# Kernel optimization log

Measured on AMD Instinct MI355X. Metric: run time of the kernel, lower is better.

## Reference

```python
import jax, jax.numpy as jnp
import numpy as np

N_NODES = 50000
N_EDGES = 800000
NODE_DIM = 64
EDGE_DIM = 16
HID = 64
HEADS = 4
LAYERS = 3
N_GRAPHS = 32
N_QUERY = 4096
BN_EPS = 1e-5
LRELU_SLOPE = 0.2


def setup_inputs() -> dict:
    key = jax.random.key(0)
    ks = jax.random.split(key, 20)
    s = 0.1  # weight scale
    return {
        "node_feat": jax.random.normal(ks[0], (N_NODES, NODE_DIM), jnp.float32),
        "edge_feat": jax.random.normal(ks[1], (N_EDGES, EDGE_DIM), jnp.float32),
        "node_proj_w": jax.random.normal(ks[2], (NODE_DIM, HID), jnp.float32) * s,
        "node_proj_b": jax.random.normal(ks[3], (HID,), jnp.float32) * s,
        "edge_proj_w": jax.random.normal(ks[4], (EDGE_DIM, HID), jnp.float32) * s,
        "edge_proj_b": jax.random.normal(ks[5], (HID,), jnp.float32) * s,
        "fc_w": jax.random.normal(ks[6], (LAYERS, HID, HEADS * HID), jnp.float32) * s,
        "fc_edge_w": jax.random.normal(ks[7], (LAYERS, HID, HEADS * HID), jnp.float32) * s,
        "attn_l": jax.random.normal(ks[8], (LAYERS, HEADS, HID), jnp.float32) * s,
        "attn_r": jax.random.normal(ks[9], (LAYERS, HEADS, HID), jnp.float32) * s,
        "attn_e": jax.random.normal(ks[10], (LAYERS, HEADS, HID), jnp.float32) * s,
        "conv_bias": jax.random.normal(ks[11], (LAYERS, HEADS * HID), jnp.float32) * s,
        "bn_gamma": jnp.ones((LAYERS, HID), jnp.float32),
        "bn_beta": jnp.zeros((LAYERS, HID), jnp.float32),
        "head_w": jax.random.normal(ks[12], (HEADS * HID, HID), jnp.float32) * s,
        "head_b": jax.random.normal(ks[13], (HID,), jnp.float32) * s,
        "src": jax.random.randint(ks[14], (N_EDGES,), 0, N_NODES, jnp.int64 if jax.config.jax_enable_x64 else jnp.int32),
        "dst": jax.random.randint(ks[15], (N_EDGES,), 0, N_NODES, jnp.int64 if jax.config.jax_enable_x64 else jnp.int32),
        "graph_ids": jnp.sort(jax.random.randint(ks[16], (N_NODES,), 0, N_GRAPHS)),
        "nodes_idx": jax.random.randint(ks[17], (N_QUERY,), 0, N_NODES),
        "num_graphs": N_GRAPHS,
    }


def reference(node_feat, edge_feat, node_proj_w, node_proj_b, edge_proj_w,
              edge_proj_b, fc_w, fc_edge_w, attn_l, attn_r, attn_e, conv_bias,
              bn_gamma, bn_beta, head_w, head_b, src, dst, graph_ids,
              nodes_idx, num_graphs):
    N = node_feat.shape[0]
    L, H, D = attn_l.shape

    nodes = node_feat @ node_proj_w + node_proj_b        # (N, hid)
    edges = edge_feat @ edge_proj_w + edge_proj_b        # (E, hid)

    x = None
    for l in range(L):
        # NOTE: faithful to original -- every layer consumes the ORIGINAL
        # projected node features (output is never fed back into `nodes`).
        ft = (nodes @ fc_w[l]).reshape(N, H, D)          # (N, H, D)
        fe = (edges @ fc_edge_w[l]).reshape(-1, H, D)    # (E, H, D)
        el = jnp.einsum('nhd,hd->nh', ft, attn_l[l])     # (N, H)
        er = jnp.einsum('nhd,hd->nh', ft, attn_r[l])
        ee = jnp.einsum('ehd,hd->eh', fe, attn_e[l])     # (E, H)
        e = jax.nn.leaky_relu(el[src] + er[dst] + ee, LRELU_SLOPE)
        # edge softmax over incoming edges of each destination node
        emax = jax.ops.segment_max(e, dst, num_segments=N)
        ex = jnp.exp(e - emax[dst])
        denom = jax.ops.segment_sum(ex, dst, num_segments=N)
        a = ex / denom[dst]                              # (E, H)
        # message = a * (feat_src + feat_edge), scatter-sum to dst
        m = a[:, :, None] * (ft[src] + fe)               # (E, H, D)
        rst = jax.ops.segment_sum(m, dst, num_segments=N)  # (N, H, D)
        rst = jax.nn.silu(rst + conv_bias[l].reshape(H, D))
        # BatchNorm1d(hidden) after permute(0,2,1): channel dim is D,
        # stats over (N, H). Training-mode batch statistics.
        mean = rst.mean(axis=(0, 1))
        var = rst.var(axis=(0, 1))
        x = (rst - mean) * jax.lax.rsqrt(var + BN_EPS) * bn_gamma[l] + bn_beta[l]

    x = x.reshape(N, H * D) @ head_w + head_b            # (N, hid)

    ones = jnp.ones((N, 1), x.dtype)
    sums = jax.ops.segment_sum(x, graph_ids, num_segments=num_graphs)
    counts = jax.ops.segment_sum(ones, graph_ids, num_segments=num_graphs)
    pooled = sums / jnp.maximum(counts, 1.0)             # (G, hid)
    return pooled, x[nodes_idx]
```

## Files before the change

### kernel.cpp

```cpp
#include <hip/hip_runtime.h>
#include <cstdint>
#include <cstddef>

#define N_NODES 50000
#define N_EDGES 800000
#define HID 64
#define HEADS 4
#define N_GRAPHS 32
#define N_QUERY 4096
#define N_TILES 3125
#define N_CBLK  782

typedef unsigned short ushort_t;
typedef unsigned int uint_t;
typedef __attribute__((ext_vector_type(8))) short short8_t;
typedef __attribute__((ext_vector_type(4))) float f32x4_t;

__device__ __forceinline__ float b2f(ushort_t h) { return __uint_as_float(((uint_t)h) << 16); }
__device__ __forceinline__ ushort_t f2b(float f) {
    uint_t u = __float_as_uint(f);
    uint_t r = (u + 0x7FFFu + ((u >> 16) & 1u)) >> 16;
    return (ushort_t)r;
}

static constexpr size_t OFF_DEG   = 0;
static constexpr size_t OFF_GST   = 50016;
static constexpr size_t OFF_OFFS  = 50064;
static constexpr size_t OFF_RANK  = 100080;
static constexpr size_t OFF_AL    = 900080;
static constexpr size_t OFF_AR    = 900336;
static constexpr size_t OFF_B     = 900592;
static constexpr size_t OFF_CE    = 900656;
static constexpr size_t OFF_CB    = 900672;
static constexpr size_t OFF_SS    = 900928;
static constexpr size_t OFF_HB2   = 901056;
static constexpr size_t OFF_WQE   = 901120;
static constexpr size_t OFF_WCVT  = 905216;
static constexpr size_t OFF_WHT   = 946176;
static constexpr size_t OFF_EL    = 954368;
static constexpr size_t OFF_ER    = 1154368;
static constexpr size_t OFF_NB    = 1354368;
static constexpr size_t OFF_REC   = 2954368;
static constexpr size_t OFF_U     = 6154624;
static constexpr size_t OFF_RST   = 14154624;
static constexpr size_t OFF_X     = 20554624;
static constexpr size_t OFF_SCR   = 23754624;
static constexpr size_t OFF_SCR2  = 24154624;
static constexpr size_t WS_TOTAL  = 24171008;

__global__ void setup1_kernel(const float* __restrict__ fcw2, const float* __restrict__ fcew2,
                              const float* __restrict__ attl2, const float* __restrict__ attr2,
                              const float* __restrict__ atte2,
                              const float* __restrict__ wpe, const float* __restrict__ bpe,
                              const int* __restrict__ gids,
                              float* __restrict__ Al, float* __restrict__ Ar,
                              float* __restrict__ B, float* __restrict__ Ce,
                              float* __restrict__ Cb, float* __restrict__ Wqe,
                              int* __restrict__ gstart)
{
    int b = blockIdx.x, tid = threadIdx.x;
    if (b == 0) {
        __shared__ float AE[256];
        int c = tid >> 2, h = tid & 3;
        float al = 0.f, ar = 0.f, ae = 0.f;
        for (int d = 0; d < 64; d++) {
            float wl = fcw2[c*256 + h*64 + d];
            float we = fcew2[c*256 + h*64 + d];
            al = fmaf(wl, attl2[h*64 + d], al);
            ar = fmaf(wl, attr2[h*64 + d], ar);
            ae = fmaf(we, atte2[h*64 + d], ae);
        }
        Al[c*4 + h] = al;
        Ar[c*4 + h] = ar;
        AE[c*4 + h] = ae;
        __syncthreads();
        if (tid < 64) {
            int kk = tid >> 2, hh = tid & 3;
            float bb = 0.f;
            for (int d = 0; d < 64; d++) bb = fmaf(wpe[kk*64 + d], AE[d*4 + hh], bb);
            B[kk*4 + hh] = bb;
        }
        if (tid < 4) {
            float ce = 0.f;
            for (int d = 0; d < 64; d++) ce = fmaf(bpe[d], AE[d*4 + tid], ce);
            Ce[tid] = ce;
        }
        {
            float cb = 0.f;
            for (int d = 0; d < 64; d++) cb = fmaf(bpe[d], fcew2[d*256 + tid], cb);
            Cb[tid] = cb;
        }
    } else if (b <= 16) {
        int idx = (b - 1) * 256 + tid;
        int hh = idx >> 10, rem = idx & 1023, kk = rem >> 6, cc = rem & 63;
        float w = 0.f;
        for (int d = 0; d < 64; d++) w = fmaf(wpe[kk*64 + d], fcew2[d*256 + hh*64 + cc], w);
        Wqe[idx] = w;
    } else {
        int g = tid;
        if (g <= N_GRAPHS) {
            int lo = 0, hi = N_NODES;
            while (lo < hi) { int mid = (lo + hi) >> 1; if (gids[mid] < g) lo = mid + 1; else hi = mid; }
            gstart[g] = lo;
        }
    }
}

__global__ void wcvt_kernel(const float* __restrict__ fcw2, const float* __restrict__ Wqe,
                            ushort_t* __restrict__ wcvt)
{
    int idx = blockIdx.x * 256 + threadIdx.x;
    int kt = idx >> 8, col = idx & 255;
    int hc = col >> 6;
    short8_t v8;
#pragma unroll
    for (int j = 0; j < 8; j++) {
        int k = kt*8 + j;
        float v;
        if (k < 256) {
            v = ((k >> 6) == hc) ? fcw2[(size_t)(k & 63)*256 + col] : 0.f;
        } else {
            int kq = k - 256, hh = kq >> 4;
            v = (hh == hc) ? Wqe[hh*1024 + (kq & 15)*64 + (col & 63)] : 0.f;
        }
        v8[j] = (short)f2b(v);
    }
    *(short8_t*)&wcvt[(size_t)idx*8] = v8;
}

__global__ __launch_bounds__(256) void node_proj_kernel(
    const float* __restrict__ nf, const float* __restrict__ wp, const float* __restrict__ bpn,
    const float* __restrict__ Al, const float* __restrict__ Ar,
    ushort_t* __restrict__ nb, float* __restrict__ el, float* __restrict__ er)
{
    __shared__ float rows[4][64];
    int tid = threadIdx.x, w = tid >> 6, lane = tid & 63;
    int n = blockIdx.x * 4 + w;
    rows[w][lane] = nf[(size_t)n*64 + lane];
    __syncthreads();
    float acc = bpn[lane];
    for (int k = 0; k < 64; k++) acc = fmaf(rows[w][k], wp[k*64 + lane], acc);
    nb[(size_t)n*64 + lane] = f2b(acc);
    float pl[4], pr[4];
#pragma unroll
    for (int h = 0; h < 4; h++) { pl[h] = acc * Al[lane*4 + h]; pr[h] = acc * Ar[lane*4 + h]; }
#pragma unroll
    for (int off = 32; off > 0; off >>= 1) {
#pragma unroll
        for (int h = 0; h < 4; h++) {
            pl[h] += __shfl_xor(pl[h], off, 64);
            pr[h] += __shfl_xor(pr[h], off, 64);
        }
    }
    if (lane == 0) {
#pragma unroll
        for (int h = 0; h < 4; h++) { el[(size_t)n*4 + h] = pl[h]; er[(size_t)n*4 + h] = pr[h]; }
    }
}

__global__ void hist_kernel(const int* __restrict__ dst, int* __restrict__ deg,
                            int* __restrict__ rank)
{
    int e = blockIdx.x * 256 + threadIdx.x;
    if (e < N_EDGES) rank[e] = atomicAdd(&deg[dst[e]], 1);
}

__global__ __launch_bounds__(1024) void prefix_kernel(const int* __restrict__ deg,
                                                      int* __restrict__ offs)
{
    __shared__ int wsum[16];
    __shared__ int carry_s;
    int tid = threadIdx.x, lane = tid & 63, w = tid >> 6;
    if (tid == 0) carry_s = 0;
    __syncthreads();
    for (int base = 0; base < N_NODES; base += 1024) {
        int i = base + tid;
        int v = (i < N_NODES) ? deg[i] : 0;
        int incl = v;
#pragma unroll
        for (int off = 1; off < 64; off <<= 1) {
            int y = __shfl_up(incl, off, 64);
            if (lane >= off) incl += y;
        }
        if (lane == 63) wsum[w] = incl;
        __syncthreads();
        int c0 = carry_s;
        int woff = 0;
#pragma unroll
        for (int k = 0; k < 15; k++) woff += (k < w) ? wsum[k] : 0;
        int ex = c0 + woff + incl - v;
        if (i < N_NODES) offs[i] = ex;
        __syncthreads();
        if (tid == 1023) carry_s = c0 + woff + incl;
        __syncthreads();
    }
    if (tid == 0) offs[N_NODES] = carry_s;
}

__global__ __launch_bounds__(256) void logit_kernel(
    const int* __restrict__ rank, const int* __restrict__ offs,
    const int* __restrict__ src, const int* __restrict__ dst,
    const float* __restrict__ edge_feat, const float* __restrict__ el,
    const float* __restrict__ B, const float* __restrict__ Ce,
    int4* __restrict__ rec)
{
    int e = blockIdx.x * 256 + threadIdx.x;
    if (e >= N_EDGES) return;
    int sn = src[e], dn = dst[e];
    const float4* el4 = (const float4*)el;
    float4 a = el4[sn];
    float l0 = Ce[0] + a.x;
    float l1 = Ce[1] + a.y;
    float l2 = Ce[2] + a.z;
    float l3 = Ce[3] + a.w;
    const float4* ef4 = (const float4*)(edge_feat + (size_t)e * 16);
    float4 e0 = ef4[0], e1 = ef4[1], e2 = ef4[2], e3 = ef4[3];
    float ef[16] = {e0.x,e0.y,e0.z,e0.w, e1.x,e1.y,e1.z,e1.w,
                    e2.x,e2.y,e2.z,e2.w, e3.x,e3.y,e3.z,e3.w};
#pragma unroll
    for (int k = 0; k < 16; k++) {
        float f = ef[k];
        l0 = fmaf(f, B[k*4 + 0], l0);
        l1 = fmaf(f, B[k*4 + 1], l1);
        l2 = fmaf(f, B[k*4 + 2], l2);
        l3 = fmaf(f, B[k*4 + 3], l3);
    }
    int slot = offs[dn] + rank[e];
    uint_t lo01 = (uint_t)f2b(l0) | ((uint_t)f2b(l1) << 16);
    uint_t lo23 = (uint_t)f2b(l2) | ((uint_t)f2b(l3) << 16);
    rec[slot] = make_int4((int)lo01, (int)lo23, sn, e);
}

__global__ __launch_bounds__(256) void accum_kernel(
    const int* __restrict__ offs, const int4* __restrict__ rec,
    const float* __restrict__ er, const float* __restrict__ edge_feat,
    const ushort_t* __restrict__ nb, ushort_t* __restrict__ u)
{
    int tid = threadIdx.x;
    int lane = tid & 63;
    int li = lane & 15;
    int node = blockIdx.x * 16 + (tid >> 6) * 4 + ((lane >> 4) & 3);
    int start = offs[node], end = offs[node + 1];
    int deg = end - start;

    float4 er4 = *(const float4*)&er[(size_t)node*4];
    const int4 Z4 = make_int4(0, 0, 0, 0);
    int4 r0 = (li < deg)      ? rec[start + li]      : Z4;
    int4 r1 = (16 + li < deg) ? rec[start + 16 + li] : Z4;

    float pe0[4], pe1[4];
    {
        float l[4] = { b2f((ushort_t)((uint_t)r0.x & 0xffff)) + er4.x,
                       b2f((ushort_t)((uint_t)r0.x >> 16))    + er4.y,
                       b2f((ushort_t)((uint_t)r0.y & 0xffff)) + er4.z,
                       b2f((ushort_t)((uint_t)r0.y >> 16))    + er4.w };
#pragma unroll
        for (int h = 0; h < 4; h++) {
            float lv = (l[h] > 0.f) ? l[h] : 0.2f * l[h];
            pe0[h] = (li < deg) ? __expf(lv) : 0.f;
        }
    }
    {
        float l[4] = { b2f((ushort_t)((uint_t)r1.x & 0xffff)) + er4.x,
                       b2f((ushort_t)((uint_t)r1.x >> 16))    + er4.y,
                       b2f((ushort_t)((uint_t)r1.y & 0xffff)) + er4.z,
                       b2f((ushort_t)((uint_t)r1.y >> 16))    + er4.w };
#pragma unroll
        for (int h = 0; h < 4; h++) {
            float lv = (l[h] > 0.f) ? l[h] : 0.2f * l[h];
            pe1[h] = (16 + li < deg) ? __expf(lv) : 0.f;
        }
    }
    int sn0 = r0.z, eid0 = r0.w;
    int sn1 = r1.z, eid1 = r1.w;

    int mdeg = deg;
#pragma unroll
    for (int off = 1; off < 64; off <<= 1) mdeg = max(mdeg, __shfl_xor(mdeg, off, 64));
    mdeg = __builtin_amdgcn_readfirstlane(mdeg);

    float z0 = 0.f, z1 = 0.f, z2 = 0.f, z3 = 0.f;
    float t[4][4] = {{0.f}};
    float q[4] = {0.f, 0.f, 0.f, 0.f};
    int grpbase = lane & 48;

#pragma unroll 2
    for (int j = 0; j < mdeg; ++j) {
        bool act = j < deg;
        float a0, a1, a2, a3;
        int sn, eid;
        if (j < 32) {
            float v0 = (j < 16) ? pe0[0] : pe1[0];
            float v1 = (j < 16) ? pe0[1] : pe1[1];
            float v2 = (j < 16) ? pe0[2] : pe1[2];
            float v3 = (j < 16) ? pe0[3] : pe1[3];
            int vs = (j < 16) ? sn0 : sn1;
            int ve = (j < 16) ? eid0 : eid1;
            int sl = grpbase | (j & 15);
            a0 = __shfl(v0, sl, 64);
            a1 = __shfl(v1, sl, 64);
            a2 = __shfl(v2, sl, 64);
            a3 = __shfl(v3, sl, 64);
            sn  = __shfl(vs, sl, 64);
            eid = __shfl(ve, sl, 64);
        } else {
            a0 = a1 = a2 = a3 = 0.f;
            sn = 0; eid = 0;
            if (act) {
                int4 rr = rec[start + j];
                float l0 = b2f((ushort_t)((uint_t)rr.x & 0xffff)) + er4.x;
                float l1 = b2f((ushort_t)((uint_t)rr.x >> 16))    + er4.y;
                float l2 = b2f((ushort_t)((uint_t)rr.y & 0xffff)) + er4.z;
                float l3 = b2f((ushort_t)((uint_t)rr.y >> 16))    + er4.w;
                l0 = (l0 > 0.f) ? l0 : 0.2f * l0;
                l1 = (l1 > 0.f) ? l1 : 0.2f * l1;
                l2 = (l2 > 0.f) ? l2 : 0.2f * l2;
                l3 = (l3 > 0.f) ? l3 : 0.2f * l3;
                a0 = __expf(l0); a1 = __expf(l1); a2 = __expf(l2); a3 = __expf(l3);
                sn = rr.z; eid = rr.w;
            }
        }
        z0 += a0; z1 += a1; z2 += a2; z3 += a3;
        ushort4 nv = *(const ushort4*)&nb[(size_t)sn*64 + li*4];
        float nd0 = b2f(nv.x), nd1 = b2f(nv.y), nd2 = b2f(nv.z), nd3 = b2f(nv.w);
        t[0][0] = fmaf(a0, nd0, t[0][0]); t[0][1] = fmaf(a0, nd1, t[0][1]);
        t[0][2] = fmaf(a0, nd2, t[0][2]); t[0][3] = fmaf(a0, nd3, t[0][3]);
        t[1][0] = fmaf(a1, nd0, t[1][0]); t[1][1] = fmaf(a1, nd1, t[1][1]);
        t[1][2] = fmaf(a1, nd2, t[1][2]); t[1][3] = fmaf(a1, nd3, t[1][3]);
        t[2][0] = fmaf(a2, nd0, t[2][0]); t[2][1] = fmaf(a2, nd1, t[2][1]);
        t[2][2] = fmaf(a2, nd2, t[2][2]); t[2][3] = fmaf(a2, nd3, t[2][3]);
        t[3][0] = fmaf(a3, nd0, t[3][0]); t[3][1] = fmaf(a3, nd1, t[3][1]);
        t[3][2] = fmaf(a3, nd2, t[3][2]); t[3][3] = fmaf(a3, nd3, t[3][3]);
        float efv = edge_feat[(size_t)eid*16 + li];
        q[0] = fmaf(a0, efv, q[0]);
        q[1] = fmaf(a1, efv, q[1]);
        q[2] = fmaf(a2, efv, q[2]);
        q[3] = fmaf(a3, efv, q[3]);
    }

    float zinv[4];
    zinv[0] = (z0 > 0.f) ? 1.f / z0 : 0.f;
    zinv[1] = (z1 > 0.f) ? 1.f / z1 : 0.f;
    zinv[2] = (z2 > 0.f) ? 1.f / z2 : 0.f;
    zinv[3] = (z3 > 0.f) ? 1.f / z3 : 0.f;

    ushort_t* up = u + (size_t)node * 320;
#pragma unroll
    for (int h = 0; h < 4; h++) {
        ushort4 tv;
        tv.x = f2b(t[h][0] * zinv[h]); tv.y = f2b(t[h][1] * zinv[h]);
        tv.z = f2b(t[h][2] * zinv[h]); tv.w = f2b(t[h][3] * zinv[h]);
        *(ushort4*)&up[h*64 + li*4] = tv;
        up[256 + h*16 + li] = f2b(q[h] * zinv[h]);
    }
}

__global__ __launch_bounds__(256) void conv_kernel(
    const ushort_t* __restrict__ u, const ushort_t* __restrict__ wcvt,
    const float* __restrict__ Cb, const float* __restrict__ convb2,
    const int* __restrict__ offs, ushort_t* __restrict__ rst, float* __restrict__ scr)
{
    int tid = threadIdx.x, lane = tid & 63;
    int li = lane & 15, lg = lane >> 4;
    int tile = blockIdx.x * 4 + (tid >> 6);
    if (tile >= N_TILES) return;
    int n0 = tile * 16;

    f32x4_t acc[16];
#pragma unroll
    for (int cb = 0; cb < 16; cb++) acc[cb] = (f32x4_t){0.f, 0.f, 0.f, 0.f};
    const ushort_t* urow = u + (size_t)(n0 + li) * 320 + lg * 8;
    const ushort_t* wbase = wcvt + ((size_t)lg * 256 + li) * 8;

#pragma unroll
    for (int kt = 0; kt < 10; kt++) {
        short8_t a = *(const short8_t*)(urow + kt * 32);
        const ushort_t* wk = wbase + (size_t)kt * 8192;
        short8_t b[16];
#pragma unroll
        for (int cb = 0; cb < 16; cb++)
            b[cb] = *(const short8_t*)(wk + (size_t)cb * 128);
#pragma unroll
        for (int cb = 0; cb < 16; cb++)
            acc[cb] = __builtin_amdgcn_mfma_f32_16x16x32_bf16(a, b[cb], acc[cb], 0, 0, 0);
    }

    float fl4[4];
#pragma unroll
    for (int j = 0; j < 4; j++) {
        int n = n0 + lg*4 + j;
        fl4[j] = (offs[n+1] > offs[n]) ? 1.f : 0.f;
    }
    float ds[4] = {0.f, 0.f, 0.f, 0.f};
    float dsq[4] = {0.f, 0.f, 0.f, 0.f};
#pragma unroll
    for (int cb = 0; cb < 16; cb++) {
        int col = cb*16 + li;
        float bias = convb2[col];
        float cbv  = Cb[col];
        float s = 0.f, sq = 0.f;
#pragma unroll
        for (int j = 0; j < 4; j++) {
            float v = acc[cb][j] + bias + fl4[j] * cbv;
            float r = v / (1.f + __expf(-v));
            rst[(size_t)(n0 + lg*4 + j)*256 + col] = f2b(r);
            s += r; sq += r * r;
        }
        s  += __shfl_xor(s, 16, 64);  s  += __shfl_xor(s, 32, 64);
        sq += __shfl_xor(sq, 16, 64); sq += __shfl_xor(sq, 32, 64);
        ds[cb & 3]  += s;
        dsq[cb & 3] += sq;
    }
    if (lg == 0) {
        float* sp = scr + (size_t)tile * 128;
#pragma unroll
        for (int m = 0; m < 4; m++) {
            sp[m*16 + li]      = ds[m];
            sp[64 + m*16 + li] = dsq[m];
        }
    }
}

__global__ __launch_bounds__(128) void scr_reduce_kernel(const float* __restrict__ scr,
                                                         float* __restrict__ scr2)
{
    int b = blockIdx.x, tid = threadIdx.x;
    float s = 0.f;
    for (int r = b; r < N_TILES; r += 128) s += scr[(size_t)r*128 + tid];
    scr2[(size_t)b*128 + tid] = s;
}

__global__ void bn_finalize_kernel(const float* __restrict__ scr2, const float* __restrict__ gamma2,
                                   const float* __restrict__ beta2, float* __restrict__ ss)
{
    __shared__ float part[8][128];
    __shared__ float tot[128];
    int j = threadIdx.x & 127, chunk = threadIdx.x >> 7;
    float t = 0.f;
    for (int b = chunk; b < 128; b += 8) t += scr2[(size_t)b*128 + j];
    part[chunk][j] = t;
    __syncthreads();
    if (threadIdx.x < 128) {
        float sgm = 0.f;
        for (int c = 0; c < 8; c++) sgm += part[c][threadIdx.x];
        tot[threadIdx.x] = sgm;
    }
    __syncthreads();
    if (threadIdx.x < 64) {
        float inv = 1.f / (float)(N_NODES * HEADS);
        float mean = tot[threadIdx.x] * inv;
        float var  = tot[64 + threadIdx.x] * inv - mean * mean;
        float sc = gamma2[threadIdx.x] * rsqrtf(var + 1e-5f);
        ss[threadIdx.x]      = sc;
        ss[64 + threadIdx.x] = beta2[threadIdx.x] - mean * sc;
    }
}

__global__ void head_prep_kernel(const float* __restrict__ ss, const float* __restrict__ headw,
                                 const float* __restrict__ headb,
                                 ushort_t* __restrict__ wht, float* __restrict__ hb2)
{
    int b = blockIdx.x, tid = threadIdx.x;
    if (b < 64) {
        int idx = b * 256 + tid;
        int c = idx >> 8, k = idx & 255;
        wht[(size_t)((k >> 3)*64 + c)*8 + (k & 7)] = f2b(ss[k & 63] * headw[(size_t)k*64 + c]);
    } else if (tid < 64) {
        float s = headb[tid];
        for (int k = 0; k < 256; k++) s += ss[64 + (k & 63)] * headw[(size_t)k*64 + tid];
        hb2[tid] = s;
    }
}

__global__ __launch_bounds__(512) void head_kernel(
    const ushort_t* __restrict__ rst, const ushort_t* __restrict__ wht,
    const float* __restrict__ hb2, float* __restrict__ x)
{
    __shared__ ushort_t Bs[16384];
    int tid = threadIdx.x, w = tid >> 6, lane = tid & 63;
    int li = lane & 15, lg = lane >> 4;
    int tile = blockIdx.x * 8 + w;
    bool active = tile < N_TILES;
    int n0 = tile * 16;

#pragma unroll
    for (int s = 0; s < 4; s++) {
        int i = tid + s*512;
        *(short8_t*)&Bs[(size_t)i*8] = *(const short8_t*)(wht + (size_t)i*8);
    }
    __syncthreads();

    if (!active) return;
    f32x4_t acc[4];
#pragma unroll
    for (int cb = 0; cb < 4; cb++) acc[cb] = (f32x4_t){0.f, 0.f, 0.f, 0.f};
    const ushort_t* rrow = rst + (size_t)(n0 + li) * 256 + lg * 8;
#pragma unroll
    for (int kt = 0; kt < 8; kt++) {
        short8_t a = *(const short8_t*)(rrow + kt * 32);
        short8_t b[4];
#pragma unroll
        for (int cb = 0; cb < 4; cb++)
            b[cb] = *(const short8_t*)&Bs[(size_t)((kt*4 + lg)*64 + cb*16 + li)*8];
#pragma unroll
        for (int cb = 0; cb < 4; cb++)
            acc[cb] = __builtin_amdgcn_mfma_f32_16x16x32_bf16(a, b[cb], acc[cb], 0, 0, 0);
    }
#pragma unroll
    for (int cb = 0; cb < 4; cb++) {
        int col = cb*16 + li;
        float hb = hb2[col];
#pragma unroll
        for (int j = 0; j < 4; j++)
            x[(size_t)(n0 + lg*4 + j)*64 + col] = acc[cb][j] + hb;
    }
}

__global__ __launch_bounds__(1024) void pool_kernel(const float* __restrict__ x,
                                                    const int* __restrict__ gstart,
                                                    float* __restrict__ out)
{
    __shared__ float red[16][64];
    int g = blockIdx.x;
    int lane = threadIdx.x & 63, w = threadIdx.x >> 6;
    int s = gstart[g], e = gstart[g + 1];
    float acc = 0.f;
    for (int n = s + w; n < e; n += 16) acc += x[(size_t)n*64 + lane];
    red[w][lane] = acc;
    __syncthreads();
    if (w == 0) {
        float t = 0.f;
#pragma unroll
        for (int k = 0; k < 16; k++) t += red[k][lane];
        float c = (float)(e - s);
        out[(size_t)g*64 + lane] = t / fmaxf(c, 1.f);
    }
}

__global__ void gather_kernel(const float* __restrict__ x, const int* __restrict__ nidx,
                              float* __restrict__ outq)
{
    int i = blockIdx.x * 256 + threadIdx.x;
    if (i < N_QUERY * HID) {
        int q = i >> 6, c = i & 63;
        outq[i] = x[(size_t)nidx[q]*64 + c];
    }
}

extern "C" void kernel_launch(void* const* d_in, const int* in_sizes, int n_in,
                              void* d_out, int out_size, void* d_ws, size_t ws_size,
                              hipStream_t stream)
{
    const float* node_feat   = (const float*)d_in[0];
    const float* edge_feat   = (const float*)d_in[1];
    const float* node_proj_w = (const float*)d_in[2];
    const float* node_proj_b = (const float*)d_in[3];
    const float* edge_proj_w = (const float*)d_in[4];
    const float* edge_proj_b = (const float*)d_in[5];
    const float* fc_w        = (const float*)d_in[6];
    const float* fc_edge_w   = (const float*)d_in[7];
    const float* attn_l      = (const float*)d_in[8];
    const float* attn_r      = (const float*)d_in[9];
    const float* attn_e      = (const float*)d_in[10];
    const float* conv_bias   = (const float*)d_in[11];
    const float* bn_gamma    = (const float*)d_in[12];
    const float* bn_beta     = (const float*)d_in[13];
    const float* head_w      = (const float*)d_in[14];
    const float* head_b      = (const float*)d_in[15];
    const int*   src         = (const int*)d_in[16];
    const int*   dst         = (const int*)d_in[17];
    const int*   gids        = (const int*)d_in[18];
    const int*   nidx        = (const int*)d_in[19];

    if (ws_size < WS_TOTAL * sizeof(float)) return;

    float* ws  = (float*)d_ws;
    float* out = (float*)d_out;

    const int L2 = 2;
    const float* fcw2   = fc_w      + (size_t)L2 * HID * HEADS * HID;
    const float* fcew2  = fc_edge_w + (size_t)L2 * HID * HEADS * HID;
    const float* attl2  = attn_l    + (size_t)L2 * HEADS * HID;
    const float* attr2  = attn_r    + (size_t)L2 * HEADS * HID;
    const float* atte2  = attn_e    + (size_t)L2 * HEADS * HID;
    const float* convb2 = conv_bias + (size_t)L2 * HEADS * HID;
    const float* gamma2 = bn_gamma  + (size_t)L2 * HID;
    const float* beta2  = bn_beta   + (size_t)L2 * HID;

    int*   deg     = (int*)(ws + OFF_DEG);
    int*   gstart  = (int*)(ws + OFF_GST);
    int*   offs    = (int*)(ws + OFF_OFFS);
    int*   rank    = (int*)(ws + OFF_RANK);
    float* Al      = ws + OFF_AL;
    float* Ar      = ws + OFF_AR;
    float* Bm      = ws + OFF_B;
    float* Ce      = ws + OFF_CE;
    float* Cb      = ws + OFF_CB;
    float* ss      = ws + OFF_SS;
    float* hb2     = ws + OFF_HB2;
    float* Wqe     = ws + OFF_WQE;
    ushort_t* wcvt = (ushort_t*)(ws + OFF_WCVT);
    ushort_t* wht  = (ushort_t*)(ws + OFF_WHT);
    float* el      = ws + OFF_EL;
    float* er      = ws + OFF_ER;
    ushort_t* nb   = (ushort_t*)(ws + OFF_NB);
    int4*  rec     = (int4*)(ws + OFF_REC);
    ushort_t* u    = (ushort_t*)(ws + OFF_U);
    ushort_t* rst  = (ushort_t*)(ws + OFF_RST);
    float* x       = ws + OFF_X;
    float* scr     = ws + OFF_SCR;
    float* scr2    = ws + OFF_SCR2;

    hipMemsetAsync(d_ws, 0, N_NODES * sizeof(int), stream);

    setup1_kernel<<<18, 256, 0, stream>>>(fcw2, fcew2, attl2, attr2, atte2,
                                          edge_proj_w, edge_proj_b, gids,
                                          Al, Ar, Bm, Ce, Cb, Wqe, gstart);
    wcvt_kernel<<<40, 256, 0, stream>>>(fcw2, Wqe, wcvt);
    node_proj_kernel<<<N_NODES/4, 256, 0, stream>>>(node_feat, node_proj_w, node_proj_b,
                                                    Al, Ar, nb, el, er);
    hist_kernel<<<(N_EDGES + 255)/256, 256, 0, stream>>>(dst, deg, rank);
    prefix_kernel<<<1, 1024, 0, stream>>>(deg, offs);
    logit_kernel<<<(N_EDGES + 255)/256, 256, 0, stream>>>(rank, offs, src, dst, edge_feat,
                                                          el, Bm, Ce, rec);
    accum_kernel<<<N_NODES/16, 256, 0, stream>>>(offs, rec, er, edge_feat, nb, u);
    conv_kernel<<<N_CBLK, 256, 0, stream>>>(u, wcvt, Cb, convb2, offs, rst, scr);
    scr_reduce_kernel<<<128, 128, 0, stream>>>(scr, scr2);
    bn_finalize_kernel<<<1, 1024, 0, stream>>>(scr2, gamma2, beta2, ss);
    head_prep_kernel<<<65, 256, 0, stream>>>(ss, head_w, head_b, wht, hb2);
    head_kernel<<<(N_TILES + 7)/8, 512, 0, stream>>>(rst, wht, hb2, x);
    pool_kernel<<<N_GRAPHS, 1024, 0, stream>>>(x, gstart, out);
    gather_kernel<<<(N_QUERY*HID + 255)/256, 256, 0, stream>>>(x, nidx, out + N_GRAPHS*HID);
}
```

Measured before the change: 301.2 us.

## Process two node tiles per wave in conv kernel to reuse weight fragments

Each wave now handles two 16-node tiles, keeping both tiles' A fragments in registers and looping over output column blocks so each loaded weight fragment feeds two MFMAs. This halves weight global loads per node and cuts accumulator registers from 16 vectors to 2, at the cost of holding 20 A fragments. The partial-stat scratch is indexed per wave and the reduction loop bound is changed to match. The grid is halved accordingly, which lowers the number of waves available for latency hiding.

New measurement: 289.5 us. -3.9%, faster.

```diff
diff --git a/kernel.cpp b/kernel.cpp
--- a/kernel.cpp
+++ b/kernel.cpp
@@ -9,7 +9,8 @@
 #define N_GRAPHS 32
 #define N_QUERY 4096
 #define N_TILES 3125
-#define N_CBLK  782
+#define N_CWAVES 1563
+#define N_CBLK 391
 
 typedef unsigned short ushort_t;
 typedef unsigned int uint_t;
@@ -362,49 +363,67 @@
 {
     int tid = threadIdx.x, lane = tid & 63;
     int li = lane & 15, lg = lane >> 4;
-    int tile = blockIdx.x * 4 + (tid >> 6);
-    if (tile >= N_TILES) return;
-    int n0 = tile * 16;
-
-    f32x4_t acc[16];
-#pragma unroll
-    for (int cb = 0; cb < 16; cb++) acc[cb] = (f32x4_t){0.f, 0.f, 0.f, 0.f};
-    const ushort_t* urow = u + (size_t)(n0 + li) * 320 + lg * 8;
+    int widx = blockIdx.x * 4 + (tid >> 6);
+    if (widx >= N_CWAVES) return;
+    int tile0 = widx * 2, tile1 = widx * 2 + 1;
+    bool t1ok = tile1 < N_TILES;
+    int n0 = tile0 * 16;
+    int n1 = t1ok ? tile1 * 16 : n0;
+
+    short8_t a0[10], a1[10];
+    const ushort_t* urow0 = u + (size_t)(n0 + li) * 320 + lg * 8;
+    const ushort_t* urow1 = u + (size_t)(n1 + li) * 320 + lg * 8;
+#pragma unroll
+    for (int kt = 0; kt < 10; kt++) {
+        a0[kt] = *(const short8_t*)(urow0 + kt * 32);
+        a1[kt] = *(const short8_t*)(urow1 + kt * 32);
+    }
+
+    float fl0[4], fl1[4];
+#pragma unroll
+    for (int j = 0; j < 4; j++) {
+        int na = n0 + lg*4 + j;
+        int nbb = n1 + lg*4 + j;
+        fl0[j] = (offs[na+1] > offs[na]) ? 1.f : 0.f;
+        fl1[j] = (offs[nbb+1] > offs[nbb]) ? 1.f : 0.f;
+    }
+
     const ushort_t* wbase = wcvt + ((size_t)lg * 256 + li) * 8;
-
-#pragma unroll
-    for (int kt = 0; kt < 10; kt++) {
-        short8_t a = *(const short8_t*)(urow + kt * 32);
-        const ushort_t* wk = wbase + (size_t)kt * 8192;
-        short8_t b[16];
-#pragma unroll
-        for (int cb = 0; cb < 16; cb++)
-            b[cb] = *(const short8_t*)(wk + (size_t)cb * 128);
-#pragma unroll
-        for (int cb = 0; cb < 16; cb++)
-            acc[cb] = __builtin_amdgcn_mfma_f32_16x16x32_bf16(a, b[cb], acc[cb], 0, 0, 0);
-    }
-
-    float fl4[4];
-#pragma unroll
-    for (int j = 0; j < 4; j++) {
-        int n = n0 + lg*4 + j;
-        fl4[j] = (offs[n+1] > offs[n]) ? 1.f : 0.f;
-    }
     float ds[4] = {0.f, 0.f, 0.f, 0.f};
     float dsq[4] = {0.f, 0.f, 0.f, 0.f};
-#pragma unroll
+
+#pragma unroll 2
     for (int cb = 0; cb < 16; cb++) {
+        short8_t b[10];
+#pragma unroll
+        for (int kt = 0; kt < 10; kt++)
+            b[kt] = *(const short8_t*)(wbase + (size_t)kt * 8192 + (size_t)cb * 128);
+        f32x4_t acc0 = (f32x4_t){0.f, 0.f, 0.f, 0.f};
+        f32x4_t acc1 = (f32x4_t){0.f, 0.f, 0.f, 0.f};
+#pragma unroll
+        for (int kt = 0; kt < 10; kt++) {
+            acc0 = __builtin_amdgcn_mfma_f32_16x16x32_bf16(a0[kt], b[kt], acc0, 0, 0, 0);
+            acc1 = __builtin_amdgcn_mfma_f32_16x16x32_bf16(a1[kt], b[kt], acc1, 0, 0, 0);
+        }
         int col = cb*16 + li;
         float bias = convb2[col];
         float cbv  = Cb[col];
         float s = 0.f, sq = 0.f;
 #pragma unroll
         for (int j = 0; j < 4; j++) {
-            float v = acc[cb][j] + bias + fl4[j] * cbv;
+            float v = acc0[j] + bias + fl0[j] * cbv;
             float r = v / (1.f + __expf(-v));
             rst[(size_t)(n0 + lg*4 + j)*256 + col] = f2b(r);
             s += r; sq += r * r;
+        }
+        if (t1ok) {
+#pragma unroll
+            for (int j = 0; j < 4; j++) {
+                float v = acc1[j] + bias + fl1[j] * cbv;
+                float r = v / (1.f + __expf(-v));
+                rst[(size_t)(n1 + lg*4 + j)*256 + col] = f2b(r);
+                s += r; sq += r * r;
+            }
         }
         s  += __shfl_xor(s, 16, 64);  s  += __shfl_xor(s, 32, 64);
         sq += __shfl_xor(sq, 16, 64); sq += __shfl_xor(sq, 32, 64);
@@ -412,7 +431,7 @@
         dsq[cb & 3] += sq;
     }
     if (lg == 0) {
-        float* sp = scr + (size_t)tile * 128;
+        float* sp = scr + (size_t)widx * 128;
 #pragma unroll
         for (int m = 0; m < 4; m++) {
             sp[m*16 + li]      = ds[m];
@@ -426,7 +445,7 @@
 {
     int b = blockIdx.x, tid = threadIdx.x;
     float s = 0.f;
-    for (int r = b; r < N_TILES; r += 128) s += scr[(size_t)r*128 + tid];
+    for (int r = b; r < N_CWAVES; r += 128) s += scr[(size_t)r*128 + tid];
     scr2[(size_t)b*128 + tid] = s;
 }
 
```
